# Kernel optimization log

Measured on AMD Instinct MI355X. Metric: run time of the kernel, lower is better.

## Reference

```python
import jax, jax.numpy as jnp
import numpy as np

B, S, D_IN = 128, 196, 512
H, DK, RATIO = 8, 32, 4
DV = RATIO * DK                      # 128
QKV_DIM = H * (2 * DK + DV)          # 1536
PROJ_IN = H * DV                     # 1024
EPS = 1e-3                           # keras BatchNormalization default epsilon
SCALE = DK ** (-0.5)


def hard_swish(x):
    return x * jnp.clip(x + 3.0, 0.0, 6.0) * (1.0 / 6.0)


def setup_inputs() -> dict:
    key = jax.random.key(0)
    ks = jax.random.split(key, 12)
    inp = {
        "x": jax.random.normal(ks[0], (B, S, D_IN), dtype=jnp.float32),
        "W_qkv": jax.random.normal(ks[1], (D_IN, QKV_DIM), dtype=jnp.float32) * (D_IN ** -0.5),
        "b_qkv": jnp.zeros((QKV_DIM,), dtype=jnp.float32),
        "gamma1": jnp.ones((QKV_DIM,), dtype=jnp.float32),
        "beta1": jnp.zeros((QKV_DIM,), dtype=jnp.float32),
        "mean1": jax.random.normal(ks[2], (QKV_DIM,), dtype=jnp.float32) * 0.1,
        "var1": jax.random.uniform(ks[3], (QKV_DIM,), minval=0.5, maxval=1.5, dtype=jnp.float32),
        "W_proj": jax.random.normal(ks[4], (PROJ_IN, D_IN), dtype=jnp.float32) * (PROJ_IN ** -0.5),
        "b_proj": jnp.zeros((D_IN,), dtype=jnp.float32),
        "gamma2": jnp.ones((D_IN,), dtype=jnp.float32),
        "beta2": jnp.zeros((D_IN,), dtype=jnp.float32),
        "mean2": jax.random.normal(ks[5], (D_IN,), dtype=jnp.float32) * 0.1,
        "var2": jax.random.uniform(ks[6], (D_IN,), minval=0.5, maxval=1.5, dtype=jnp.float32),
    }
    return inp


def _bn(x, gamma, beta, mean, var):
    # inference-mode BatchNorm over the last (channel) axis
    return (x - mean) * jax.lax.rsqrt(var + EPS) * gamma + beta


def reference(x, W_qkv, b_qkv, gamma1, beta1, mean1, var1,
              W_proj, b_proj, gamma2, beta2, mean2, var2):
    # QKV projection + BN
    qkv = _bn(x @ W_qkv + b_qkv, gamma1, beta1, mean1, var1)      # [B,S,1536]
    qkv = qkv.reshape(B, S, H, 2 * DK + DV)
    q, k, v = jnp.split(qkv, [DK, 2 * DK], axis=3)                # [B,S,H,*]
    q = jnp.transpose(q, (0, 2, 1, 3))                            # [B,H,S,DK]
    k = jnp.transpose(k, (0, 2, 1, 3))
    v = jnp.transpose(v, (0, 2, 1, 3))                            # [B,H,S,DV]
    attn = jax.nn.softmax(jnp.einsum("bhqd,bhkd->bhqk", q, k) * SCALE, axis=-1)
    av = jnp.einsum("bhqk,bhkd->bhqd", attn, v)                   # [B,H,S,DV]
    # faithful to original: transpose to [B,H,DV,S] then reshape to [B,S,H*DV]
    hidden = jnp.transpose(av, (0, 1, 3, 2)).reshape(B, S, PROJ_IN)
    hidden = hard_swish(hidden)
    out = _bn(hidden @ W_proj + b_proj, gamma2, beta2, mean2, var2)  # [B,S,512]
    return out
```

## Files before the change

### kernel.cpp

```cpp
#include <hip/hip_runtime.h>
#include <math.h>

namespace {

constexpr int Bb   = 128;
constexpr int Ss   = 196;
constexpr int DIN  = 512;
constexpr int Hh   = 8;
constexpr int DKc  = 32;
constexpr int DVc  = 128;
constexpr int QKVD = 1536;
constexpr int PIN  = 1024;
constexpr int Mrows = Bb * Ss;
constexpr float EPSc   = 1e-3f;
constexpr float SCALEc = 0.17677669529663687f;

typedef __bf16 bf16x8 __attribute__((ext_vector_type(8)));
typedef __bf16 bf16x4 __attribute__((ext_vector_type(4)));
typedef float  f32x4  __attribute__((ext_vector_type(4)));

constexpr int VT_STRIDE = 232;
constexpr size_t VT_QELEMS = 8192;
constexpr size_t VT_BH = 4 * VT_QELEMS;

__device__ __forceinline__ void gl_lds16(const void* g, void* l) {
    __builtin_amdgcn_global_load_lds(
        (const __attribute__((address_space(1))) void*)g,
        (__attribute__((address_space(3))) void*)l, 16, 0, 0);
}

__global__ __launch_bounds__(256)
void prep(const float* __restrict__ W1, __bf16* __restrict__ WT1o,
          const float* __restrict__ W2, __bf16* __restrict__ WT2o,
          const float* __restrict__ x, __bf16* __restrict__ xb)
{
    int id = blockIdx.x;
    if (id >= 1280) {
        const int i = (id - 1280) * 256 + threadIdx.x;
        float4 v = ((const float4*)x)[i];
        bf16x4 o = { (__bf16)v.x, (__bf16)v.y, (__bf16)v.z, (__bf16)v.w };
        ((bf16x4*)xb)[i] = o;
        return;
    }
    __shared__ float tile[32][33];
    const float* W; __bf16* WT; int K, N, bx, by;
    if (id < 768) { W = W1; WT = WT1o; K = 512;  N = 1536; bx = id % 48; by = id / 48; }
    else { id -= 768; W = W2; WT = WT2o; K = 1024; N = 512;  bx = id % 16; by = id / 16; }
    const int n0 = bx * 32, k0 = by * 32;
    const int tx = threadIdx.x & 31, ty = threadIdx.x >> 5;
#pragma unroll
    for (int i = ty; i < 32; i += 8)
        tile[i][tx] = W[(size_t)(k0 + i) * N + n0 + tx];
    __syncthreads();
#pragma unroll
    for (int i = ty; i < 32; i += 8)
        WT[(size_t)(n0 + i) * K + k0 + tx] = (__bf16)tile[tx][i];
}

__global__ __launch_bounds__(512)
void gemm1_bn_scatter(const __bf16* __restrict__ A, const __bf16* __restrict__ BT,
                      const float* __restrict__ bias, const float* __restrict__ gamma,
                      const float* __restrict__ beta, const float* __restrict__ mean,
                      const float* __restrict__ var,
                      __bf16* __restrict__ qkvO, __bf16* __restrict__ VTp)
{
    constexpr int K = DIN;
    __shared__ __align__(16) char sm[147456];

    const int t    = threadIdx.x;
    const int wid  = t >> 6;
    const int lane = t & 63;
    const int lr   = lane & 15;
    const int q    = lane >> 4;

    constexpr int ntiles = 6;
    constexpr int nwg = 196 * ntiles;
    const int bid = (blockIdx.x & 7) * (nwg >> 3) + (blockIdx.x >> 3);
    const int m0 = (bid / ntiles) * 128;
    const int n0 = (bid % ntiles) * 256;
    const int wm  = (wid & 1) * 64;
    const int wnL = (wid >> 1) * 64;

    char* ring0 = sm;
    char* ring1 = sm + 49152;
    char* ring2 = sm + 98304;
    char* rings[3] = { ring0, ring1, ring2 };

    auto STAGE = [&](int kt, char* rg) {
#pragma unroll
        for (int e = 0; e < 2; ++e) {
            const int c = e * 512 + t;
            const int gsrc = (c & 7) ^ ((c >> 3) & 7);
            gl_lds16(A + (size_t)(m0 + (c >> 3)) * K + kt * 64 + gsrc * 8,
                     rg + c * 16);
        }
#pragma unroll
        for (int e = 0; e < 4; ++e) {
            const int c = e * 512 + t;
            const int gsrc = (c & 7) ^ ((c >> 3) & 7);
            gl_lds16(BT + (size_t)(n0 + (c >> 3)) * K + kt * 64 + gsrc * 8,
                     rg + 16384 + c * 16);
        }
    };

    f32x4 acc[4][4] = {};

    STAGE(0, ring0);
    STAGE(1, ring1);
    asm volatile("s_waitcnt vmcnt(6)" ::: "memory");
    __builtin_amdgcn_s_barrier();
    __builtin_amdgcn_sched_barrier(0);

#pragma unroll
    for (int p = 0; p < 8; ++p) {
        if (p <= 5) STAGE(p + 2, rings[(p + 2) % 3]);
        const char* rg = rings[p % 3];

        bf16x8 aF[2][4], bF[2][4];
#pragma unroll
        for (int kh = 0; kh < 2; ++kh) {
#pragma unroll
            for (int i = 0; i < 4; ++i) {
                const int row = wm + i * 16 + lr;
                const int off = row * 128 + (((kh * 4 + q) ^ (row & 7)) << 4);
                aF[kh][i] = *(const bf16x8*)(rg + off);
            }
#pragma unroll
            for (int j = 0; j < 4; ++j) {
                const int row = wnL + j * 16 + lr;
                const int off = 16384 + row * 128 + (((kh * 4 + q) ^ (row & 7)) << 4);
                bF[kh][j] = *(const bf16x8*)(rg + off);
            }
        }
        __builtin_amdgcn_s_setprio(1);
#pragma unroll
        for (int kh = 0; kh < 2; ++kh)
#pragma unroll
            for (int i = 0; i < 4; ++i)
#pragma unroll
                for (int j = 0; j < 4; ++j)
                    acc[i][j] = __builtin_amdgcn_mfma_f32_16x16x32_bf16(
                        aF[kh][i], bF[kh][j], acc[i][j], 0, 0, 0);
        __builtin_amdgcn_s_setprio(0);

        if (p <= 5)      asm volatile("s_waitcnt vmcnt(6)" ::: "memory");
        else if (p == 6) asm volatile("s_waitcnt vmcnt(0)" ::: "memory");
        __builtin_amdgcn_s_barrier();
        __builtin_amdgcn_sched_barrier(0);
    }

    char* wsl = sm + wid * 16384;
    const int g64   = (n0 >> 6) + (wid >> 1);
    const bool isQK = (g64 % 3) == 0;
    const int h     = g64 / 3;
    const int nbase = n0 + (wid >> 1) * 64;
    const int mbase = m0 + (wid & 1) * 64;

    if (isQK) {
        __bf16* qk = (__bf16*)wsl;
#pragma unroll
        for (int j = 0; j < 4; ++j) {
            const int n = nbase + j * 16 + lr;
            const float s  = gamma[n] * rsqrtf(var[n] + EPSc);
            const float tv = fmaf(bias[n] - mean[n], s, beta[n]);
#pragma unroll
            for (int i = 0; i < 4; ++i)
#pragma unroll
                for (int r = 0; r < 4; ++r)
                    qk[(i * 16 + q * 4 + r) * 72 + j * 16 + lr] =
                        (__bf16)fmaf(acc[i][j][r], s, tv);
        }
#pragma unroll
        for (int rr = 0; rr < 8; ++rr) {
            const int row = rr * 8 + (lane >> 3);
            const int g   = lane & 7;
            bf16x8 vv = *(const bf16x8*)(qk + row * 72 + g * 8);
            *(bf16x8*)(qkvO + (size_t)(mbase + row) * QKVD + nbase + g * 8) = vv;
        }
    } else {
        __bf16* vr = (__bf16*)wsl;
        const int d0 = nbase - h * 192 - 64;
#pragma unroll
        for (int j = 0; j < 4; ++j) {
            const int n = nbase + j * 16 + lr;
            const float s  = gamma[n] * rsqrtf(var[n] + EPSc);
            const float tv = fmaf(bias[n] - mean[n], s, beta[n]);
#pragma unroll
            for (int i = 0; i < 4; ++i) {
                bf16x4 pk = { (__bf16)fmaf(acc[i][j][0], s, tv),
                              (__bf16)fmaf(acc[i][j][1], s, tv),
                              (__bf16)fmaf(acc[i][j][2], s, tv),
                              (__bf16)fmaf(acc[i][j][3], s, tv) };
                *(bf16x4*)(vr + (j * 16 + lr) * 72 + i * 16 + q * 4) = pk;
            }
        }
#pragma unroll
        for (int rr = 0; rr < 8; ++rr) {
            const int idx  = rr * 64 + lane;
            const int colL = idx >> 3;
            const int r0   = (idx & 7) * 8;
            const int d    = d0 + colL;
            const int mrow = mbase + r0;
            const int b_   = mrow / 196;
            const int s0   = mrow - b_ * 196;
            __bf16* dst0 = VTp + (size_t)(b_ * 8 + h) * VT_BH
                         + (size_t)(d >> 5) * VT_QELEMS + (size_t)(d & 31) * VT_STRIDE;
            bf16x8 vv = *(const bf16x8*)(vr + colL * 72 + r0);
            if (s0 <= 188) {
                *(bf16x8*)(dst0 + s0) = vv;
            } else {
#pragma unroll
                for (int e = 0; e < 8; ++e) {
                    int se = s0 + e;
                    __bf16* dst = dst0;
                    if (se >= 196) { se -= 196; dst += 8 * VT_BH; }
                    dst[se] = vv[e];
                }
            }
        }
    }
}

template<int N, int K>
__global__ __launch_bounds__(256)
void gemm_bn_mfma(const __bf16* __restrict__ A, const __bf16* __restrict__ BT,
                  const float* __restrict__ bias, const float* __restrict__ gamma,
                  const float* __restrict__ beta, const float* __restrict__ mean,
                  const float* __restrict__ var, float* __restrict__ C)
{
    constexpr int BM = 128, BN = 128;
    __shared__ __align__(16) char sm[65536];
    const int t    = threadIdx.x;
    const int wave = t >> 6;
    const int lane = t & 63;
    const int lr   = lane & 15;
    const int q    = lane >> 4;
    constexpr int ntiles = N / BN;
    constexpr int nwg = 196 * ntiles;
    const int bid = (blockIdx.x & 7) * (nwg >> 3) + (blockIdx.x >> 3);
    const int m0 = (bid / ntiles) * BM;
    const int n0 = (bid % ntiles) * BN;
    const int wm = (wave & 1) * 64;
    const int wn = (wave >> 1) * 64;
    const __bf16* aG0 = A  + (size_t)(m0 + (t >> 2)) * K + (t & 3) * 8;
    const __bf16* aG1 = aG0 + (size_t)64 * K;
    const __bf16* bG0 = BT + (size_t)(n0 + (t >> 2)) * K + (t & 3) * 8;
    const __bf16* bG1 = bG0 + (size_t)64 * K;

    auto STAGE = [&](int k0, int cur) {
        char* lA = sm + cur * 16384 + wave * 1024;
        char* lB = sm + 32768 + cur * 16384 + wave * 1024;
        gl_lds16(aG0 + k0,      lA);
        gl_lds16(aG1 + k0,      lA + 4096);
        gl_lds16(aG0 + k0 + 32, lA + 8192);
        gl_lds16(aG1 + k0 + 32, lA + 8192 + 4096);
        gl_lds16(bG0 + k0,      lB);
        gl_lds16(bG1 + k0,      lB + 4096);
        gl_lds16(bG0 + k0 + 32, lB + 8192);
        gl_lds16(bG1 + k0 + 32, lB + 8192 + 4096);
    };

    f32x4 acc[4][4] = {};

    STAGE(0, 0);
    __syncthreads();
    int cur = 0;
    for (int k0 = 0; k0 < K; k0 += 64) {
        if (k0 + 64 < K) STAGE(k0 + 64, cur ^ 1);
        const __bf16* Abuf = (const __bf16*)(sm + cur * 16384);
        const __bf16* Bbuf = (const __bf16*)(sm + 32768 + cur * 16384);
#pragma unroll
        for (int kk = 0; kk < 2; ++kk) {
            bf16x8 aF[4], bF[4];
#pragma unroll
            for (int i = 0; i < 4; ++i)
                aF[i] = *(const bf16x8*)(Abuf + kk * 4096 + (wm + i * 16 + lr) * 32 + q * 8);
#pragma unroll
            for (int j = 0; j < 4; ++j)
                bF[j] = *(const bf16x8*)(Bbuf + kk * 4096 + (wn + j * 16 + lr) * 32 + q * 8);
#pragma unroll
            for (int i = 0; i < 4; ++i)
#pragma unroll
                for (int j = 0; j < 4; ++j)
                    acc[i][j] = __builtin_amdgcn_mfma_f32_16x16x32_bf16(
                        aF[i], bF[j], acc[i][j], 0, 0, 0);
        }
        __syncthreads();
        cur ^= 1;
    }
#pragma unroll
    for (int j = 0; j < 4; ++j) {
        const int n = n0 + wn + j * 16 + lr;
        const float s  = gamma[n] * rsqrtf(var[n] + EPSc);
        const float tv = fmaf(bias[n] - mean[n], s, beta[n]);
#pragma unroll
        for (int i = 0; i < 4; ++i) {
            const int mrow = m0 + wm + i * 16 + q * 4;
#pragma unroll
            for (int r = 0; r < 4; ++r)
                C[(size_t)(mrow + r) * N + n] = fmaf(acc[i][j][r], s, tv);
        }
    }
}

__global__ __launch_bounds__(1024)
void attn_mfma(const __bf16* __restrict__ qkv, const __bf16* __restrict__ VTp,
               __bf16* __restrict__ hidden)
{
    __shared__ __align__(16) char smem[145920];
    __bf16* Kb = (__bf16*)smem;

    const int t = threadIdx.x;
    const int wave = t >> 6, lane = t & 63;
    const int lr = lane & 15, q = lane >> 4;
    const int bh = blockIdx.x;
    const int b = bh >> 3, h = bh & 7;
    const __bf16* qkvb = qkv + (size_t)b * 196 * QKVD + h * 192;

    const char* gV = (const char*)(VTp + (size_t)bh * VT_BH);
    char* ldsV = smem + 113152;
    gl_lds16(gV + wave * 1024 + lane * 16, ldsV + wave * 1024);

    if (t < 196 * 4) {
        const int s = t >> 2, c = t & 3;
        bf16x8 v = *(const bf16x8*)(qkvb + (size_t)s * QKVD + 32 + c * 8);
        *(bf16x8*)(Kb + s * 40 + c * 8) = v;
    }

    __syncthreads();

    const int qt = wave;
    const bool wactive = (qt <= 12);
    __bf16* Pw = (__bf16*)(smem + 16640 + (wactive ? qt : 0) * 7424);

    if (wactive) {
        int sQ = qt * 16 + lr; if (sQ > 195) sQ = 195;
        bf16x8 aQ = *(const bf16x8*)(qkv + ((size_t)b * 196 + sQ) * QKVD + h * 192 + q * 8);

        f32x4 sc[13];
#pragma unroll
        for (int nt = 0; nt < 13; ++nt) {
            bf16x8 bK = *(const bf16x8*)(Kb + (nt * 16 + lr) * 40 + q * 8);
            f32x4 z = {0.f, 0.f, 0.f, 0.f};
            sc[nt] = __builtin_amdgcn_mfma_f32_16x16x32_bf16(aQ, bK, z, 0, 0, 0);
        }
        float mrow[4] = {-1e30f, -1e30f, -1e30f, -1e30f};
#pragma unroll
        for (int nt = 0; nt < 13; ++nt) {
            const bool valid = (nt < 12) | (lr < 4);
#pragma unroll
            for (int r = 0; r < 4; ++r) {
                float x = sc[nt][r] * SCALEc;
                sc[nt][r] = x;
                if (valid) mrow[r] = fmaxf(mrow[r], x);
            }
        }
#pragma unroll
        for (int d = 1; d < 16; d <<= 1)
#pragma unroll
            for (int r = 0; r < 4; ++r)
                mrow[r] = fmaxf(mrow[r], __shfl_xor(mrow[r], d, 64));
        float l[4] = {0.f, 0.f, 0.f, 0.f};
#pragma unroll
        for (int nt = 0; nt < 13; ++nt) {
            const bool valid = (nt < 12) | (lr < 4);
#pragma unroll
            for (int r = 0; r < 4; ++r) {
                float e = valid ? __expf(sc[nt][r] - mrow[r]) : 0.f;
                sc[nt][r] = e;
                l[r] += e;
            }
        }
#pragma unroll
        for (int d = 1; d < 16; d <<= 1)
#pragma unroll
            for (int r = 0; r < 4; ++r)
                l[r] += __shfl_xor(l[r], d, 64);
        float inv[4];
#pragma unroll
        for (int r = 0; r < 4; ++r) inv[r] = 1.f / l[r];

#pragma unroll
        for (int nt = 0; nt < 13; ++nt)
#pragma unroll
            for (int r = 0; r < 4; ++r)
                Pw[(q * 4 + r) * 232 + nt * 16 + lr] = (__bf16)(sc[nt][r] * inv[r]);
        for (int idx = lane; idx < 16 * 24; idx += 64) {
            int row = idx & 15, cz = 208 + (idx >> 4);
            Pw[row * 232 + cz] = (__bf16)0.f;
        }
    }

    const int sbase = qt * 16 + q * 4;
    const bool sval = wactive && (sbase + 3 < 196);
    __bf16* hb = hidden + (size_t)b * 200704 + (size_t)h * 25088;

    for (int q4 = 0; q4 < 4; ++q4) {
        const __bf16* Vl = (const __bf16*)(ldsV + (q4 & 1) * 16384);
        if (q4 < 3)
            gl_lds16(gV + (size_t)(q4 + 1) * 16384 + wave * 1024 + lane * 16,
                     ldsV + ((q4 + 1) & 1) * 16384 + wave * 1024);
        if (wactive) {
            f32x4 o0 = {0.f, 0.f, 0.f, 0.f}, o1 = {0.f, 0.f, 0.f, 0.f};
#pragma unroll
            for (int kk = 0; kk < 7; ++kk) {
                bf16x8 aP = *(const bf16x8*)(Pw + lr * 232 + kk * 32 + q * 8);
                bf16x8 b0 = *(const bf16x8*)(Vl + lr * 232 + kk * 32 + q * 8);
                bf16x8 b1 = *(const bf16x8*)(Vl + (16 + lr) * 232 + kk * 32 + q * 8);
                o0 = __builtin_amdgcn_mfma_f32_16x16x32_bf16(aP, b0, o0, 0, 0, 0);
                o1 = __builtin_amdgcn_mfma_f32_16x16x32_bf16(aP, b1, o1, 0, 0, 0);
            }
            if (sval) {
#pragma unroll
                for (int nt2 = 0; nt2 < 2; ++nt2) {
                    f32x4 o = nt2 ? o1 : o0;
                    const int d = q4 * 32 + nt2 * 16 + lr;
                    bf16x4 pk;
#pragma unroll
                    for (int r = 0; r < 4; ++r) {
                        float x = o[r];
                        pk[r] = (__bf16)(x * fminf(fmaxf(x + 3.f, 0.f), 6.f) * (1.f / 6.f));
                    }
                    *(bf16x4*)(hb + (size_t)d * 196 + sbase) = pk;
                }
            }
        }
        if (q4 < 3) __syncthreads();
    }
}

}

extern "C" void kernel_launch(void* const* d_in, const int* in_sizes, int n_in,
                              void* d_out, int out_size, void* d_ws, size_t ws_size,
                              hipStream_t stream)
{
    const float* x    = (const float*)d_in[0];
    const float* Wqkv = (const float*)d_in[1];
    const float* bqkv = (const float*)d_in[2];
    const float* g1   = (const float*)d_in[3];
    const float* be1  = (const float*)d_in[4];
    const float* mu1  = (const float*)d_in[5];
    const float* va1  = (const float*)d_in[6];
    const float* Wp   = (const float*)d_in[7];
    const float* bp   = (const float*)d_in[8];
    const float* g2   = (const float*)d_in[9];
    const float* be2  = (const float*)d_in[10];
    const float* mu2  = (const float*)d_in[11];
    const float* va2  = (const float*)d_in[12];

    char* ws = (char*)d_ws;
    __bf16* qkv    = (__bf16*)ws;
    __bf16* VTp    = (__bf16*)(ws + 77070336);
    __bf16* hidden = (__bf16*)(ws + 144179200);
    __bf16* xb     = (__bf16*)(ws + 195559424);
    __bf16* WT1    = (__bf16*)(ws + 221249536);
    __bf16* WT2    = (__bf16*)(ws + 222822400);
    float*  out    = (float*)d_out;

    prep<<<dim3(13824), dim3(256), 0, stream>>>(Wqkv, WT1, Wp, WT2, x, xb);

    gemm1_bn_scatter<<<dim3(196 * 6), dim3(512), 0, stream>>>(
        xb, WT1, bqkv, g1, be1, mu1, va1, qkv, VTp);

    attn_mfma<<<dim3(Bb * Hh), dim3(1024), 0, stream>>>(qkv, VTp, hidden);

    gemm_bn_mfma<DIN, PIN><<<dim3(196 * (DIN / 128)), dim3(256), 0, stream>>>(
        hidden, WT2, bp, g2, be2, mu2, va2, out);
}
```

Before: 263.5 us.

## Rewrite projection GEMM as 3-stage LDS ring with swizzle and 128x256 tiles

Replaces the double-buffered 128x128 projection GEMM with a 512-thread kernel on 128x256 tiles, fed by a three-slot LDS ring that prefetches two K-steps ahead. Completion is tracked with explicit vmcnt waits and raw barriers. LDS rows are XOR-swizzled to avoid bank conflicts, and the MFMA section runs at raised wave priority. The aim is to hide global-load latency and improve data reuse, at the cost of 144KB of LDS per block (one block per CU) and fewer workgroups (392).

```diff
diff --git a/kernel.cpp b/kernel.cpp
--- a/kernel.cpp
+++ b/kernel.cpp
@@ -221,76 +221,99 @@
     }
 }
 
-template<int N, int K>
-__global__ __launch_bounds__(256)
-void gemm_bn_mfma(const __bf16* __restrict__ A, const __bf16* __restrict__ BT,
-                  const float* __restrict__ bias, const float* __restrict__ gamma,
-                  const float* __restrict__ beta, const float* __restrict__ mean,
-                  const float* __restrict__ var, float* __restrict__ C)
+__global__ __launch_bounds__(512)
+void gemm2_ring(const __bf16* __restrict__ A, const __bf16* __restrict__ BT,
+                const float* __restrict__ bias, const float* __restrict__ gamma,
+                const float* __restrict__ beta, const float* __restrict__ mean,
+                const float* __restrict__ var, float* __restrict__ C)
 {
-    constexpr int BM = 128, BN = 128;
-    __shared__ __align__(16) char sm[65536];
+    constexpr int K = PIN;
+    constexpr int N = DIN;
+    constexpr int NP = K / 64;
+    __shared__ __align__(16) char sm[147456];
+
     const int t    = threadIdx.x;
-    const int wave = t >> 6;
+    const int wid  = t >> 6;
     const int lane = t & 63;
     const int lr   = lane & 15;
     const int q    = lane >> 4;
-    constexpr int ntiles = N / BN;
+
+    constexpr int ntiles = 2;
     constexpr int nwg = 196 * ntiles;
     const int bid = (blockIdx.x & 7) * (nwg >> 3) + (blockIdx.x >> 3);
-    const int m0 = (bid / ntiles) * BM;
-    const int n0 = (bid % ntiles) * BN;
-    const int wm = (wave & 1) * 64;
-    const int wn = (wave >> 1) * 64;
-    const __bf16* aG0 = A  + (size_t)(m0 + (t >> 2)) * K + (t & 3) * 8;
-    const __bf16* aG1 = aG0 + (size_t)64 * K;
-    const __bf16* bG0 = BT + (size_t)(n0 + (t >> 2)) * K + (t & 3) * 8;
-    const __bf16* bG1 = bG0 + (size_t)64 * K;
-
-    auto STAGE = [&](int k0, int cur) {
-        char* lA = sm + cur * 16384 + wave * 1024;
-        char* lB = sm + 32768 + cur * 16384 + wave * 1024;
-        gl_lds16(aG0 + k0,      lA);
-        gl_lds16(aG1 + k0,      lA + 4096);
-        gl_lds16(aG0 + k0 + 32, lA + 8192);
-        gl_lds16(aG1 + k0 + 32, lA + 8192 + 4096);
-        gl_lds16(bG0 + k0,      lB);
-        gl_lds16(bG1 + k0,      lB + 4096);
-        gl_lds16(bG0 + k0 + 32, lB + 8192);
-        gl_lds16(bG1 + k0 + 32, lB + 8192 + 4096);
+    const int m0 = (bid / ntiles) * 128;
+    const int n0 = (bid % ntiles) * 256;
+    const int wm  = (wid & 1) * 64;
+    const int wnL = (wid >> 1) * 64;
+
+    char* rings[3] = { sm, sm + 49152, sm + 98304 };
+
+    auto STAGE = [&](int kt, char* rg) {
+#pragma unroll
+        for (int e = 0; e < 2; ++e) {
+            const int c = e * 512 + t;
+            const int gsrc = (c & 7) ^ ((c >> 3) & 7);
+            gl_lds16(A + (size_t)(m0 + (c >> 3)) * K + kt * 64 + gsrc * 8,
+                     rg + c * 16);
+        }
+#pragma unroll
+        for (int e = 0; e < 4; ++e) {
+            const int c = e * 512 + t;
+            const int gsrc = (c & 7) ^ ((c >> 3) & 7);
+            gl_lds16(BT + (size_t)(n0 + (c >> 3)) * K + kt * 64 + gsrc * 8,
+                     rg + 16384 + c * 16);
+        }
     };
 
     f32x4 acc[4][4] = {};
 
-    STAGE(0, 0);
-    __syncthreads();
-    int cur = 0;
-    for (int k0 = 0; k0 < K; k0 += 64) {
-        if (k0 + 64 < K) STAGE(k0 + 64, cur ^ 1);
-        const __bf16* Abuf = (const __bf16*)(sm + cur * 16384);
-        const __bf16* Bbuf = (const __bf16*)(sm + 32768 + cur * 16384);
-#pragma unroll
-        for (int kk = 0; kk < 2; ++kk) {
-            bf16x8 aF[4], bF[4];
-#pragma unroll
-            for (int i = 0; i < 4; ++i)
-                aF[i] = *(const bf16x8*)(Abuf + kk * 4096 + (wm + i * 16 + lr) * 32 + q * 8);
-#pragma unroll
-            for (int j = 0; j < 4; ++j)
-                bF[j] = *(const bf16x8*)(Bbuf + kk * 4096 + (wn + j * 16 + lr) * 32 + q * 8);
+    STAGE(0, rings[0]);
+    STAGE(1, rings[1]);
+    asm volatile("s_waitcnt vmcnt(6)" ::: "memory");
+    __builtin_amdgcn_s_barrier();
+    __builtin_amdgcn_sched_barrier(0);
+
+#pragma unroll
+    for (int p = 0; p < NP; ++p) {
+        if (p <= NP - 3) STAGE(p + 2, rings[(p + 2) % 3]);
+        const char* rg = rings[p % 3];
+
+        bf16x8 aF[2][4], bF[2][4];
+#pragma unroll
+        for (int kh = 0; kh < 2; ++kh) {
+#pragma unroll
+            for (int i = 0; i < 4; ++i) {
+                const int row = wm + i * 16 + lr;
+                const int off = row * 128 + (((kh * 4 + q) ^ (row & 7)) << 4);
+                aF[kh][i] = *(const bf16x8*)(rg + off);
+            }
+#pragma unroll
+            for (int j = 0; j < 4; ++j) {
+                const int row = wnL + j * 16 + lr;
+                const int off = 16384 + row * 128 + (((kh * 4 + q) ^ (row & 7)) << 4);
+                bF[kh][j] = *(const bf16x8*)(rg + off);
+            }
+        }
+        __builtin_amdgcn_s_setprio(1);
+#pragma unroll
+        for (int kh = 0; kh < 2; ++kh)
 #pragma unroll
             for (int i = 0; i < 4; ++i)
 #pragma unroll
                 for (int j = 0; j < 4; ++j)
                     acc[i][j] = __builtin_amdgcn_mfma_f32_16x16x32_bf16(
-                        aF[i], bF[j], acc[i][j], 0, 0, 0);
-        }
-        __syncthreads();
-        cur ^= 1;
-    }
+                        aF[kh][i], bF[kh][j], acc[i][j], 0, 0, 0);
+        __builtin_amdgcn_s_setprio(0);
+
+        if (p <= NP - 3)      asm volatile("s_waitcnt vmcnt(6)" ::: "memory");
+        else if (p == NP - 2) asm volatile("s_waitcnt vmcnt(0)" ::: "memory");
+        __builtin_amdgcn_s_barrier();
+        __builtin_amdgcn_sched_barrier(0);
+    }
+
 #pragma unroll
     for (int j = 0; j < 4; ++j) {
-        const int n = n0 + wn + j * 16 + lr;
+        const int n = n0 + wnL + j * 16 + lr;
         const float s  = gamma[n] * rsqrtf(var[n] + EPSc);
         const float tv = fmaf(bias[n] - mean[n], s, beta[n]);
 #pragma unroll
@@ -465,6 +488,6 @@
 
     attn_mfma<<<dim3(Bb * Hh), dim3(1024), 0, stream>>>(qkv, VTp, hidden);
 
-    gemm_bn_mfma<DIN, PIN><<<dim3(196 * (DIN / 128)), dim3(256), 0, stream>>>(
+    gemm2_ring<<<dim3(196 * 2), dim3(512), 0, stream>>>(
         hidden, WT2, bp, g2, be2, mu2, va2, out);
 }
```

After: 269.0 us. 1.02x slower.
